# Kernel tuning notes

Measured on AMD Instinct MI355X. Metric: run time of the kernel, lower is better.

## Reference

```python
import jax, jax.numpy as jnp
import numpy as np

ANNEAL = 0.01

def _tsig(x, temp=ANNEAL):
    # temperature sigmoid with +/-50 clipping as in the torch source
    return jax.nn.sigmoid(jnp.clip(x / temp, -50.0, 50.0))

def setup_inputs() -> dict:
    key = jax.random.key(0)
    k1, k2 = jax.random.split(key)
    N, D = 512, 512
    preds = jax.random.normal(k1, (N, D), dtype=jnp.float32)
    labels = jax.random.randint(k2, (N,), 0, 64, dtype=jnp.int64)
    return {"preds": preds, "labels": labels}

def reference(preds, labels):
    N = preds.shape[0]
    dtype = preds.dtype
    eye = jnp.eye(N, dtype=dtype)
    same = (labels[:, None] == labels[None, :]).astype(dtype)
    I_pos = same * (1.0 - eye)                      # positives excl. self
    sim_mat = preds @ preds.T                       # [N, N]
    # sim_diff[i, j, k] = sim_mat[i, k] - sim_mat[i, j]
    sim_sg = _tsig(sim_mat[:, None, :] - sim_mat[:, :, None]) * (1.0 - eye)[None, :, :]
    sim_all_rk = 1.0 + jnp.sum(sim_sg, axis=-1)     # [N, N]
    # sum_k sim_sg[i,j,k] * I_pos[i,k]
    pos_sum = jnp.einsum('ijk,ik->ij', sim_sg, I_pos)
    sim_pos_rk = eye + I_pos + I_pos * pos_sum      # [N, N]
    n_pos = jnp.sum(I_pos, axis=1) + 1.0            # [N]
    per_anchor = jnp.sum(sim_pos_rk / sim_all_rk, axis=1) / n_pos
    per_anchor = jnp.where(n_pos > 1.0, per_anchor, 0.0)  # skip anchors with no positives
    ap = jnp.sum(per_anchor) / N
    return 1.0 - ap
```

## Files before the change

kernel.cpp:

```cpp
#include <hip/hip_runtime.h>
#include <hip/hip_bf16.h>

#define NN 512
#define BK 64

__global__ __launch_bounds__(256) void sap_gemm(const float* __restrict__ P,
                                                float* __restrict__ S,
                                                float* __restrict__ g_acc,
                                                unsigned int* __restrict__ g_cnt) {
    __shared__ float As[BK][34];
    __shared__ float Bs[BK][34];
    const int t  = threadIdx.x;
    const int tx = t & 15, ty = t >> 4;
    const int i0 = blockIdx.y * 32, j0 = blockIdx.x * 32;

    if (blockIdx.x == 0 && blockIdx.y == 0 && t == 0) { *g_acc = 0.f; *g_cnt = 0u; }

    const int lr = t >> 3;
    const int lc = (t & 7) * 4;

    float acc00 = 0.f, acc01 = 0.f, acc10 = 0.f, acc11 = 0.f;

    for (int kt = 0; kt < NN; kt += BK) {
        float4 a0 = *(const float4*)&P[(i0 + lr) * NN + kt + lc];
        float4 a1 = *(const float4*)&P[(i0 + lr) * NN + kt + lc + 32];
        float4 b0 = *(const float4*)&P[(j0 + lr) * NN + kt + lc];
        float4 b1 = *(const float4*)&P[(j0 + lr) * NN + kt + lc + 32];
        __syncthreads();
        As[lc + 0][lr] = a0.x;  As[lc + 1][lr] = a0.y;
        As[lc + 2][lr] = a0.z;  As[lc + 3][lr] = a0.w;
        As[lc + 32][lr] = a1.x; As[lc + 33][lr] = a1.y;
        As[lc + 34][lr] = a1.z; As[lc + 35][lr] = a1.w;
        Bs[lc + 0][lr] = b0.x;  Bs[lc + 1][lr] = b0.y;
        Bs[lc + 2][lr] = b0.z;  Bs[lc + 3][lr] = b0.w;
        Bs[lc + 32][lr] = b1.x; Bs[lc + 33][lr] = b1.y;
        Bs[lc + 34][lr] = b1.z; Bs[lc + 35][lr] = b1.w;
        __syncthreads();
#pragma unroll
        for (int kk = 0; kk < BK; kk++) {
            float2 av = *(const float2*)&As[kk][2 * ty];
            float2 bv = *(const float2*)&Bs[kk][2 * tx];
            acc00 += av.x * bv.x; acc01 += av.x * bv.y;
            acc10 += av.y * bv.x; acc11 += av.y * bv.y;
        }
    }
    const int i = i0 + 2 * ty, j = j0 + 2 * tx;
    S[i * NN + j]           = acc00;
    S[i * NN + j + 1]       = acc01;
    S[(i + 1) * NN + j]     = acc10;
    S[(i + 1) * NN + j + 1] = acc11;
}

__global__ __launch_bounds__(256) void sap_rows(const float* __restrict__ S,
                                               const int* __restrict__ labels,
                                               float* __restrict__ g_acc,
                                               unsigned int* __restrict__ g_cnt,
                                               float* __restrict__ out) {
    __shared__ float srow[NN];
    __shared__ float posf[NN];
    __shared__ int   poslist[NN];
    __shared__ int   npos_cnt;
    __shared__ float wave_part[4];

    const int i = blockIdx.x;
    const int t = threadIdx.x;
    if (t == 0) npos_cnt = 0;
    __syncthreads();

    const int li = labels[i];
    for (int k = t; k < NN; k += 256) {
        srow[k] = S[i * NN + k];
        bool p  = (labels[k] == li) && (k != i);
        posf[k] = p ? 1.f : 0.f;
        if (p) {
            int idx = atomicAdd(&npos_cnt, 1);
            poslist[idx] = k;
        }
    }
    __syncthreads();

    const int cnt  = npos_cnt;
    const int wave = t >> 6, lane = t & 63;
    const float C1   = 100.0f * 1.44269504088896340736f;
    const float CLIP = 50.0f * 1.44269504088896340736f;

    float acc = 0.f;
    if (cnt > 0) {
        for (int idx = wave; idx <= cnt; idx += 4) {
            const int   j   = (idx == cnt) ? i : poslist[idx];
            const float sij = srow[j];
            float sum_all = 0.f, sum_pos = 0.f;
#pragma unroll
            for (int kk = 0; kk < 8; kk++) {
                const int k = lane + (kk << 6);
                float y = (sij - srow[k]) * C1;
                y = fminf(fmaxf(y, -CLIP), CLIP);
                float tt = 1.0f / (1.0f + exp2f(y));
                if (k == j) tt = 0.f;
                sum_all += tt;
                sum_pos += tt * posf[k];
            }
#pragma unroll
            for (int off = 32; off; off >>= 1) {
                sum_all += __shfl_down(sum_all, off);
                sum_pos += __shfl_down(sum_pos, off);
            }
            if (lane == 0) {
                const float den = 1.0f + sum_all;
                const float num = (j == i) ? 1.0f : (1.0f + sum_pos);
                acc += num / den;
            }
        }
    }
    if (lane == 0) wave_part[wave] = acc;
    __syncthreads();
    if (t == 0) {
        float block_val = 0.f;
        if (cnt > 0) {
            float tot = wave_part[0] + wave_part[1] + wave_part[2] + wave_part[3];
            block_val = tot / (float)(cnt + 1);
        }
        atomicAdd(g_acc, block_val);
        __threadfence();
        unsigned int done = atomicAdd(g_cnt, 1u);
        if (done == NN - 1) {
            float total = atomicAdd(g_acc, 0.0f);
            out[0] = 1.0f - total / (float)NN;
        }
    }
}

extern "C" void kernel_launch(void* const* d_in, const int* in_sizes, int n_in,
                              void* d_out, int out_size, void* d_ws, size_t ws_size,
                              hipStream_t stream) {
    const float* preds  = (const float*)d_in[0];
    const int*   labels = (const int*)d_in[1];
    float* out = (float*)d_out;

    float*        S     = (float*)d_ws;
    float*        g_acc = (float*)d_ws + NN * NN;
    unsigned int* g_cnt = (unsigned int*)((float*)d_ws + NN * NN + 1);

    dim3 ggrid(NN / 32, NN / 32);
    sap_gemm<<<ggrid, 256, 0, stream>>>(preds, S, g_acc, g_cnt);
    sap_rows<<<NN, 256, 0, stream>>>(S, labels, g_acc, g_cnt, out);
}
```

Measured before the change: 83.22 us.

## Rework similarity GEMM with 4x4 register tiles and double-buffered shared memory

```diff
diff --git a/kernel.cpp b/kernel.cpp
--- a/kernel.cpp
+++ b/kernel.cpp
@@ -2,53 +2,87 @@
 #include <hip/hip_bf16.h>
 
 #define NN 512
-#define BK 64
+#define PITCH 34
 
-__global__ __launch_bounds__(256) void sap_gemm(const float* __restrict__ P,
-                                                float* __restrict__ S,
-                                                float* __restrict__ g_acc,
-                                                unsigned int* __restrict__ g_cnt) {
-    __shared__ float As[BK][34];
-    __shared__ float Bs[BK][34];
+__global__ __launch_bounds__(64) void sap_gemm(const float* __restrict__ P,
+                                               float* __restrict__ S,
+                                               float* __restrict__ g_acc,
+                                               unsigned int* __restrict__ g_cnt) {
+    __shared__ float As[2][32][PITCH];
+    __shared__ float Bs[2][32][PITCH];
     const int t  = threadIdx.x;
-    const int tx = t & 15, ty = t >> 4;
+    const int tx = t & 7, ty = t >> 3;
     const int i0 = blockIdx.y * 32, j0 = blockIdx.x * 32;
 
     if (blockIdx.x == 0 && blockIdx.y == 0 && t == 0) { *g_acc = 0.f; *g_cnt = 0u; }
 
-    const int lr = t >> 3;
-    const int lc = (t & 7) * 4;
+    const int srow = t >> 3;
+    const int scol = (t & 7) * 4;
 
-    float acc00 = 0.f, acc01 = 0.f, acc10 = 0.f, acc11 = 0.f;
+    float4 a_reg[4], b_reg[4];
+#pragma unroll
+    for (int p = 0; p < 4; p++) {
+        a_reg[p] = *(const float4*)&P[(i0 + srow + 8 * p) * NN + scol];
+        b_reg[p] = *(const float4*)&P[(j0 + srow + 8 * p) * NN + scol];
+    }
+#pragma unroll
+    for (int p = 0; p < 4; p++) {
+        *(float2*)&As[0][srow + 8 * p][scol]     = make_float2(a_reg[p].x, a_reg[p].y);
+        *(float2*)&As[0][srow + 8 * p][scol + 2] = make_float2(a_reg[p].z, a_reg[p].w);
+        *(float2*)&Bs[0][srow + 8 * p][scol]     = make_float2(b_reg[p].x, b_reg[p].y);
+        *(float2*)&Bs[0][srow + 8 * p][scol + 2] = make_float2(b_reg[p].z, b_reg[p].w);
+    }
 
-    for (int kt = 0; kt < NN; kt += BK) {
-        float4 a0 = *(const float4*)&P[(i0 + lr) * NN + kt + lc];
-        float4 a1 = *(const float4*)&P[(i0 + lr) * NN + kt + lc + 32];
-        float4 b0 = *(const float4*)&P[(j0 + lr) * NN + kt + lc];
-        float4 b1 = *(const float4*)&P[(j0 + lr) * NN + kt + lc + 32];
-        __syncthreads();
-        As[lc + 0][lr] = a0.x;  As[lc + 1][lr] = a0.y;
-        As[lc + 2][lr] = a0.z;  As[lc + 3][lr] = a0.w;
-        As[lc + 32][lr] = a1.x; As[lc + 33][lr] = a1.y;
-        As[lc + 34][lr] = a1.z; As[lc + 35][lr] = a1.w;
-        Bs[lc + 0][lr] = b0.x;  Bs[lc + 1][lr] = b0.y;
-        Bs[lc + 2][lr] = b0.z;  Bs[lc + 3][lr] = b0.w;
-        Bs[lc + 32][lr] = b1.x; Bs[lc + 33][lr] = b1.y;
-        Bs[lc + 34][lr] = b1.z; Bs[lc + 35][lr] = b1.w;
+    float acc[4][4] = {};
+
+    for (int c = 0; c < 16; c++) {
+        const int cur = c & 1;
+        if (c < 15) {
+            const int kt = (c + 1) * 32;
+#pragma unroll
+            for (int p = 0; p < 4; p++) {
+                a_reg[p] = *(const float4*)&P[(i0 + srow + 8 * p) * NN + kt + scol];
+                b_reg[p] = *(const float4*)&P[(j0 + srow + 8 * p) * NN + kt + scol];
+            }
+        }
         __syncthreads();
 #pragma unroll
-        for (int kk = 0; kk < BK; kk++) {
-            float2 av = *(const float2*)&As[kk][2 * ty];
-            float2 bv = *(const float2*)&Bs[kk][2 * tx];
-            acc00 += av.x * bv.x; acc01 += av.x * bv.y;
-            acc10 += av.y * bv.x; acc11 += av.y * bv.y;
+        for (int kk = 0; kk < 32; kk += 4) {
+            float4 ar[4], bc[4];
+#pragma unroll
+            for (int r = 0; r < 4; r++) {
+                float2 alo = *(const float2*)&As[cur][4 * ty + r][kk];
+                float2 ahi = *(const float2*)&As[cur][4 * ty + r][kk + 2];
+                float2 blo = *(const float2*)&Bs[cur][4 * tx + r][kk];
+                float2 bhi = *(const float2*)&Bs[cur][4 * tx + r][kk + 2];
+                ar[r] = make_float4(alo.x, alo.y, ahi.x, ahi.y);
+                bc[r] = make_float4(blo.x, blo.y, bhi.x, bhi.y);
+            }
+#pragma unroll
+            for (int r = 0; r < 4; r++)
+#pragma unroll
+                for (int cc = 0; cc < 4; cc++)
+                    acc[r][cc] += ar[r].x * bc[cc].x + ar[r].y * bc[cc].y
+                                + ar[r].z * bc[cc].z + ar[r].w * bc[cc].w;
+        }
+        if (c < 15) {
+            __syncthreads();
+            const int nxt = cur ^ 1;
+#pragma unroll
+            for (int p = 0; p < 4; p++) {
+                *(float2*)&As[nxt][srow + 8 * p][scol]     = make_float2(a_reg[p].x, a_reg[p].y);
+                *(float2*)&As[nxt][srow + 8 * p][scol + 2] = make_float2(a_reg[p].z, a_reg[p].w);
+                *(float2*)&Bs[nxt][srow + 8 * p][scol]     = make_float2(b_reg[p].x, b_reg[p].y);
+                *(float2*)&Bs[nxt][srow + 8 * p][scol + 2] = make_float2(b_reg[p].z, b_reg[p].w);
+            }
         }
     }
-    const int i = i0 + 2 * ty, j = j0 + 2 * tx;
-    S[i * NN + j]           = acc00;
-    S[i * NN + j + 1]       = acc01;
-    S[(i + 1) * NN + j]     = acc10;
-    S[(i + 1) * NN + j + 1] = acc11;
+
+#pragma unroll
+    for (int r = 0; r < 4; r++) {
+        float4 v = make_float4(acc[r][0], acc[r][1], acc[r][2], acc[r][3]);
+        *(float4*)&S[(i0 + 4 * ty + r) * NN + j0 + 4 * tx] = v;
+    }
 }
 
 __global__ __launch_bounds__(256) void sap_rows(const float* __restrict__ S,
@@ -142,6 +176,6 @@
     unsigned int* g_cnt = (unsigned int*)((float*)d_ws + NN * NN + 1);
 
     dim3 ggrid(NN / 32, NN / 32);
-    sap_gemm<<<ggrid, 256, 0, stream>>>(preds, S, g_acc, g_cnt);
+    sap_gemm<<<ggrid, 64, 0, stream>>>(preds, S, g_acc, g_cnt);
     sap_rows<<<NN, 256, 0, stream>>>(S, labels, g_acc, g_cnt, out);
 }
```

Result: slower. 96.18 us (+15.6%).

## Split-K GEMM with 64x64 swizzled tiles and fast sigmoid intrinsics

Applied to the files above, without the earlier changes.

```diff
diff --git a/kernel.cpp b/kernel.cpp
--- a/kernel.cpp
+++ b/kernel.cpp
@@ -2,56 +2,63 @@
 #include <hip/hip_bf16.h>
 
 #define NN 512
-#define BK 64
 
 __global__ __launch_bounds__(256) void sap_gemm(const float* __restrict__ P,
-                                                float* __restrict__ S,
+                                                float* __restrict__ Sp,
                                                 float* __restrict__ g_acc,
                                                 unsigned int* __restrict__ g_cnt) {
-    __shared__ float As[BK][34];
-    __shared__ float Bs[BK][34];
+    __shared__ float4 As4[64 * 32];
+    __shared__ float4 Bs4[64 * 32];
     const int t  = threadIdx.x;
-    const int tx = t & 15, ty = t >> 4;
-    const int i0 = blockIdx.y * 32, j0 = blockIdx.x * 32;
+    const int i0 = blockIdx.y * 64, j0 = blockIdx.x * 64;
+    const int kz = blockIdx.z, kbase = kz * 128;
 
-    if (blockIdx.x == 0 && blockIdx.y == 0 && t == 0) { *g_acc = 0.f; *g_cnt = 0u; }
+    if (i0 == 0 && j0 == 0 && kz == 0 && t == 0) { *g_acc = 0.f; *g_cnt = 0u; }
 
-    const int lr = t >> 3;
-    const int lc = (t & 7) * 4;
-
-    float acc00 = 0.f, acc01 = 0.f, acc10 = 0.f, acc11 = 0.f;
-
-    for (int kt = 0; kt < NN; kt += BK) {
-        float4 a0 = *(const float4*)&P[(i0 + lr) * NN + kt + lc];
-        float4 a1 = *(const float4*)&P[(i0 + lr) * NN + kt + lc + 32];
-        float4 b0 = *(const float4*)&P[(j0 + lr) * NN + kt + lc];
-        float4 b1 = *(const float4*)&P[(j0 + lr) * NN + kt + lc + 32];
-        __syncthreads();
-        As[lc + 0][lr] = a0.x;  As[lc + 1][lr] = a0.y;
-        As[lc + 2][lr] = a0.z;  As[lc + 3][lr] = a0.w;
-        As[lc + 32][lr] = a1.x; As[lc + 33][lr] = a1.y;
-        As[lc + 34][lr] = a1.z; As[lc + 35][lr] = a1.w;
-        Bs[lc + 0][lr] = b0.x;  Bs[lc + 1][lr] = b0.y;
-        Bs[lc + 2][lr] = b0.z;  Bs[lc + 3][lr] = b0.w;
-        Bs[lc + 32][lr] = b1.x; Bs[lc + 33][lr] = b1.y;
-        Bs[lc + 34][lr] = b1.z; Bs[lc + 35][lr] = b1.w;
-        __syncthreads();
+    {
+        const int col4 = t & 31;
+        const int row0 = t >> 5;
 #pragma unroll
-        for (int kk = 0; kk < BK; kk++) {
-            float2 av = *(const float2*)&As[kk][2 * ty];
-            float2 bv = *(const float2*)&Bs[kk][2 * tx];
-            acc00 += av.x * bv.x; acc01 += av.x * bv.y;
-            acc10 += av.y * bv.x; acc11 += av.y * bv.y;
+        for (int p = 0; p < 8; p++) {
+            const int row = row0 + 8 * p;
+            const float4 av = *(const float4*)&P[(i0 + row) * NN + kbase + col4 * 4];
+            const float4 bv = *(const float4*)&P[(j0 + row) * NN + kbase + col4 * 4];
+            const int c4s = (col4 & 24) | ((col4 & 7) ^ ((row >> 2) & 7));
+            As4[row * 32 + c4s] = av;
+            Bs4[row * 32 + c4s] = bv;
         }
     }
-    const int i = i0 + 2 * ty, j = j0 + 2 * tx;
-    S[i * NN + j]           = acc00;
-    S[i * NN + j + 1]       = acc01;
-    S[(i + 1) * NN + j]     = acc10;
-    S[(i + 1) * NN + j + 1] = acc11;
+    __syncthreads();
+
+    const int tx = t & 15, ty = t >> 4;
+    float acc[4][4] = {};
+
+#pragma unroll 4
+    for (int g = 0; g < 32; g++) {
+        const int ga = (g & 24) | ((g & 7) ^ (ty & 7));
+        const int gb = (g & 24) | ((g & 7) ^ (tx & 7));
+        float4 a[4], b[4];
+#pragma unroll
+        for (int r = 0; r < 4; r++) a[r] = As4[(4 * ty + r) * 32 + ga];
+#pragma unroll
+        for (int c = 0; c < 4; c++) b[c] = Bs4[(4 * tx + c) * 32 + gb];
+#pragma unroll
+        for (int r = 0; r < 4; r++)
+#pragma unroll
+            for (int c = 0; c < 4; c++)
+                acc[r][c] += a[r].x * b[c].x + a[r].y * b[c].y
+                           + a[r].z * b[c].z + a[r].w * b[c].w;
+    }
+
+    float* Sk = Sp + kz * NN * NN;
+#pragma unroll
+    for (int r = 0; r < 4; r++) {
+        float4 v = make_float4(acc[r][0], acc[r][1], acc[r][2], acc[r][3]);
+        *(float4*)&Sk[(i0 + 4 * ty + r) * NN + j0 + 4 * tx] = v;
+    }
 }
 
-__global__ __launch_bounds__(256) void sap_rows(const float* __restrict__ S,
+__global__ __launch_bounds__(256) void sap_rows(const float* __restrict__ Sp,
                                                const int* __restrict__ labels,
                                                float* __restrict__ g_acc,
                                                unsigned int* __restrict__ g_cnt,
@@ -69,7 +76,9 @@
 
     const int li = labels[i];
     for (int k = t; k < NN; k += 256) {
-        srow[k] = S[i * NN + k];
+        const int base = i * NN + k;
+        float v = Sp[base] + Sp[NN * NN + base] + Sp[2 * NN * NN + base] + Sp[3 * NN * NN + base];
+        srow[k] = v;
         bool p  = (labels[k] == li) && (k != i);
         posf[k] = p ? 1.f : 0.f;
         if (p) {
@@ -95,7 +104,7 @@
                 const int k = lane + (kk << 6);
                 float y = (sij - srow[k]) * C1;
                 y = fminf(fmaxf(y, -CLIP), CLIP);
-                float tt = 1.0f / (1.0f + exp2f(y));
+                float tt = __builtin_amdgcn_rcpf(1.0f + __builtin_amdgcn_exp2f(y));
                 if (k == j) tt = 0.f;
                 sum_all += tt;
                 sum_pos += tt * posf[k];
@@ -137,11 +146,11 @@
     const int*   labels = (const int*)d_in[1];
     float* out = (float*)d_out;
 
-    float*        S     = (float*)d_ws;
-    float*        g_acc = (float*)d_ws + NN * NN;
-    unsigned int* g_cnt = (unsigned int*)((float*)d_ws + NN * NN + 1);
+    float*        Sp    = (float*)d_ws;
+    float*        g_acc = (float*)d_ws + 4 * NN * NN;
+    unsigned int* g_cnt = (unsigned int*)((float*)d_ws + 4 * NN * NN + 1);
 
-    dim3 ggrid(NN / 32, NN / 32);
-    sap_gemm<<<ggrid, 256, 0, stream>>>(preds, S, g_acc, g_cnt);
-    sap_rows<<<NN, 256, 0, stream>>>(S, labels, g_acc, g_cnt, out);
+    dim3 ggrid(NN / 64, NN / 64, 4);
+    sap_gemm<<<ggrid, 256, 0, stream>>>(preds, Sp, g_acc, g_cnt);
+    sap_rows<<<NN, 256, 0, stream>>>(Sp, labels, g_acc, g_cnt, out);
 }
```

Result: faster. 80.44 us (-3.3%).
